# Kernel optimization log

Hardware: AMD Instinct MI355X
Metric: run time of the kernel (lower is better)

Reference implementation:

```python
import jax, jax.numpy as jnp
import numpy as np

N_INST = 1_000_000
N_BINS_X = 512
N_BINS_Y = 512
STDDEV_X = 0.6
STDDEV_Y = 0.6
STDDEV_TRUNC = 2.5
NUM_CKSR = 48
NUM_CE = 96
SLICE_CAP = 16
SQRT2 = float(np.sqrt(2.0))
# truncated window spans 2*trunc*stddev = 3.0 bin units -> at most 5 bins per axis
K = 5


def setup_inputs() -> dict:
    key = jax.random.key(0)
    k1, k2, k3, k4, k5 = jax.random.split(key, 5)
    scale = jnp.array([N_BINS_X, N_BINS_Y], dtype=jnp.float32)
    inst_pos = jax.random.uniform(k1, (N_INST, 2), dtype=jnp.float32) * scale
    luts = jax.random.randint(k2, (N_INST,), 0, 7, dtype=jnp.int32)
    luts = jnp.where(luts == 1, 0, luts)  # assert: no LUT has type 1
    ffs = jax.random.randint(k3, (N_INST,), 0, 2, dtype=jnp.int32)
    ffs = jnp.where(luts > 0, 0, ffs)  # an instance is either a LUT or a FF
    cksr = jax.random.randint(k4, (N_INST,), 0, NUM_CKSR, dtype=jnp.int32)
    ce = jax.random.randint(k5, (N_INST,), 0, NUM_CE, dtype=jnp.int32)
    ff_ctrlsets = jnp.stack([cksr, ce], axis=1)
    return {"inst_pos": inst_pos, "is_inst_luts": luts, "is_inst_ffs": ffs,
            "ff_ctrlsets": ff_ctrlsets}


def _axis_weights(pos, stddev, num_bins):
    """Truncated-Gaussian bin overlap weights along one axis.
    pos: (N,) centers in bin units. Returns bins (N,K) int32, weights (N,K)."""
    half = STDDEV_TRUNC * stddev
    lo_bin = jnp.floor(pos - half).astype(jnp.int32)            # (N,)
    bins = lo_bin[:, None] + jnp.arange(K, dtype=jnp.int32)     # (N,K)
    e_lo = bins.astype(pos.dtype)
    e_hi = e_lo + 1.0
    w_lo = (pos - half)[:, None]
    w_hi = (pos + half)[:, None]
    lo_c = jnp.clip(e_lo, w_lo, w_hi)
    hi_c = jnp.clip(e_hi, w_lo, w_hi)
    phi = lambda e: 0.5 * (1.0 + jax.lax.erf((e - pos[:, None]) / (stddev * SQRT2)))
    w = phi(hi_c) - phi(lo_c)
    valid = (bins >= 0) & (bins < num_bins)
    w = jnp.where(valid, w, 0.0)
    w = w / (jnp.sum(w, axis=1, keepdims=True) + 1e-12)  # each inst contributes unit demand
    return jnp.clip(bins, 0, num_bins - 1), w


def reference(inst_pos, is_inst_luts, is_inst_ffs, ff_ctrlsets):
    dt = inst_pos.dtype
    bx, wx = _axis_weights(inst_pos[:, 0], STDDEV_X, N_BINS_X)
    by, wy = _axis_weights(inst_pos[:, 1], STDDEV_Y, N_BINS_Y)
    w2 = wx[:, :, None] * wy[:, None, :]                        # (N,K,K)
    idx = bx[:, :, None] * N_BINS_Y + by[:, None, :]            # (N,K,K) flat bin id
    nb = N_BINS_X * N_BINS_Y

    lut_mask = is_inst_luts > 0
    ff_mask = (is_inst_ffs > 0) & (~lut_mask)

    # LUT demand map (Gaussian splat of LUT instances)
    lut_w = jnp.where(lut_mask[:, None, None], w2, 0.0)
    lut_dem = jnp.zeros(nb, dt).at[idx.reshape(-1)].add(lut_w.reshape(-1))

    # FF demand maps keyed by control sets (cksr shared per half-slice, ce per quarter)
    ff_w = jnp.where(ff_mask[:, None, None], w2, 0.0)
    cksr = ff_ctrlsets[:, 0]
    ce = ff_ctrlsets[:, 1]
    idx_ck = (idx * NUM_CKSR + cksr[:, None, None]).reshape(-1)
    idx_ce = (idx * NUM_CE + ce[:, None, None]).reshape(-1)
    ck_dem = jnp.zeros(nb * NUM_CKSR, dt).at[idx_ck].add(ff_w.reshape(-1))
    ck_dem = ck_dem.reshape(nb, NUM_CKSR)
    ce_dem = jnp.zeros(nb * NUM_CE, dt).at[idx_ce].add(ff_w.reshape(-1))
    ce_dem = ce_dem.reshape(nb, NUM_CE)

    # ultrascale packing rule: half-slice shares CK/SR, quarter-slice shares CE
    half_cap = SLICE_CAP / 2.0
    quarter_cap = SLICE_CAP / 4.0
    eff_ck = jnp.sum(jnp.ceil(ck_dem / half_cap), axis=1) * half_cap
    eff_ce = jnp.sum(jnp.ceil(ce_dem / quarter_cap), axis=1) * quarter_cap
    ff_eff = jnp.maximum(eff_ck, eff_ce)        # effective FF capacity consumed per bin
    ff_raw = jnp.sum(ck_dem, axis=1)            # raw FF demand per bin
    ff_scale = jnp.maximum(ff_eff / jnp.maximum(ff_raw, 1e-6), 1.0)
    lut_scale = jnp.maximum(lut_dem / SLICE_CAP, 1.0)

    # gather per-instance inflated resource area with the same Gaussian weights
    lut_area = jnp.sum(w2 * lut_scale[idx], axis=(1, 2))
    ff_area = jnp.sum(w2 * ff_scale[idx], axis=(1, 2))
    zero = jnp.zeros((), dt)
    return jnp.where(lut_mask, lut_area, zero) + jnp.where(ff_mask, ff_area, zero)
```

## Files before the change

kernel.cpp:

```cpp
#include <hip/hip_runtime.h>

#define N_INST   1000000
#define NBX      512
#define NBY      512
#define NB       (NBX * NBY)
#define NUM_CKSR 48
#define NUM_CE   96
#define K        4

#define FTX   16
#define FTY   8
#define TGX   (NBX / FTX)
#define TGY   (NBY / FTY)
#define NFT   (TGX * TGY)
#define CAPL  512
#define CAPF  256
#define RS    145
#define ACCW  (FTX * FTY * RS)
#define PXW   20
#define PYW   12

#define CSTRIDE 16

#define KHALF  ((float)(2.5 * 0.6))
#define KDENOM ((float)(0.6 * 1.4142135623730951))

__device__ __forceinline__ void axis_weights4(float pos, int nbins, int& lo_out, float w[K]) {
    float wlo = pos - KHALF;
    float whi = pos + KHALF;
    int lo_bin = (int)floorf(wlo);
    lo_out = lo_bin;
    float phi[K + 1];
#pragma unroll
    for (int k = 0; k <= K; ++k) {
        float e = (float)(lo_bin + k);
        float ec = fminf(fmaxf(e, wlo), whi);
        phi[k] = 0.5f * (1.f + erff((ec - pos) / KDENOM));
    }
    float wsum = 0.f;
#pragma unroll
    for (int k = 0; k < K; ++k) {
        int b = lo_bin + k;
        float ww = phi[k + 1] - phi[k];
        if (b < 0 || b >= nbins) ww = 0.f;
        w[k] = ww;
        wsum += ww;
    }
    float d = wsum + 1e-12f;
#pragma unroll
    for (int k = 0; k < K; ++k) w[k] = w[k] / d;
}

__global__ void __launch_bounds__(256) classify_kernel(
        const float* __restrict__ pos,
        const int* __restrict__ luts,
        const int* __restrict__ ffs,
        const int* __restrict__ ctrl,
        int* __restrict__ lut_cur,
        int* __restrict__ ff_cur,
        float2* __restrict__ lutb,
        uint4* __restrict__ ffb) {
    int i = blockIdx.x * blockDim.x + threadIdx.x;
    if (i >= N_INST) return;
    bool is_lut = luts[i] > 0;
    bool is_ff  = !is_lut && (ffs[i] > 0);
    if (!is_lut && !is_ff) return;

    float px = pos[2 * i], py = pos[2 * i + 1];

    if (is_lut) {
        int t = (((int)px) >> 4) * TGY + (((int)py) >> 3);
        int slot = atomicAdd(&lut_cur[t * CSTRIDE], 1);
        if (slot < CAPL) lutb[(size_t)t * CAPL + slot] = make_float2(px, py);
        return;
    }

    unsigned meta = (unsigned)ctrl[2 * i] | (((unsigned)ctrl[2 * i + 1] + 48u) << 8);
    uint4 entry = make_uint4(__float_as_uint(px), __float_as_uint(py), meta, 0u);
    int lox = (int)floorf(px - KHALF);
    int loy = (int)floorf(py - KHALF);
    int tx0 = max(lox, 0) >> 4, tx1 = min(lox + 3, NBX - 1) >> 4;
    int ty0 = max(loy, 0) >> 3, ty1 = min(loy + 3, NBY - 1) >> 3;
    for (int tx = tx0; tx <= tx1; ++tx) {
        for (int ty = ty0; ty <= ty1; ++ty) {
            int t = tx * TGY + ty;
            int slot = atomicAdd(&ff_cur[t * CSTRIDE], 1);
            if (slot < CAPF) ffb[(size_t)t * CAPF + slot] = entry;
        }
    }
}

__global__ void __launch_bounds__(1024) tile_kernel(
        const float2* __restrict__ lutb,
        const uint4* __restrict__ ffb,
        const int* __restrict__ lut_cur,
        const int* __restrict__ ff_cur,
        float* __restrict__ lut_dem,
        float* __restrict__ ff_scale) {
    __shared__ float acc[ACCW];
    __shared__ unsigned patch[PXW * PYW];
    int t = blockIdx.x;
    int X0 = (t / TGY) * FTX;
    int Y0 = (t % TGY) * FTY;
    int tid = threadIdx.x;

    for (int j = tid; j < ACCW; j += 1024) acc[j] = 0.f;
    if (tid < PXW * PYW) patch[tid] = 0u;
    __syncthreads();

    int nl = min(lut_cur[t * CSTRIDE], CAPL);
    for (int e = tid; e < nl; e += 1024) {
        float2 p = lutb[(size_t)t * CAPL + e];
        int lox, loy;
        float wx[K], wy[K];
        axis_weights4(p.x, NBX, lox, wx);
        axis_weights4(p.y, NBY, loy, wy);
        int base = (lox - (X0 - 2)) * PYW + (loy - (Y0 - 2));
#pragma unroll
        for (int kx = 0; kx < K; ++kx) {
            float wv = wx[kx] * 65536.f;
            int rb = base + kx * PYW;
#pragma unroll
            for (int ky = 0; ky < K; ++ky)
                atomicAdd(&patch[rb + ky], (unsigned)rintf(wv * wy[ky]));
        }
    }

    int nf = min(ff_cur[t * CSTRIDE], CAPF);
    for (int e = tid; e < nf; e += 1024) {
        uint4 a = ffb[(size_t)t * CAPF + e];
        float px = __uint_as_float(a.x);
        float py = __uint_as_float(a.y);
        int ck   = (int)(a.z & 255u);
        int ce48 = (int)((a.z >> 8) & 255u);
        int lox, loy;
        float wx[K], wy[K];
        axis_weights4(px, NBX, lox, wx);
        axis_weights4(py, NBY, loy, wy);
        int cx = lox - X0, cy = loy - Y0;
#pragma unroll
        for (int kx = 0; kx < K; ++kx) {
            int gx = cx + kx;
            if ((unsigned)gx >= FTX) continue;
            float wv = wx[kx];
#pragma unroll
            for (int ky = 0; ky < K; ++ky) {
                int gy = cy + ky;
                if ((unsigned)gy >= FTY) continue;
                float w2 = wv * wy[ky];
                if (w2 != 0.f) {
                    float* row = acc + (gx * FTY + gy) * RS;
                    unsafeAtomicAdd(row + ck, w2);
                    unsafeAtomicAdd(row + ce48, w2);
                }
            }
        }
    }
    __syncthreads();

    if (tid < 512) {
        int lb = tid >> 2, q = tid & 3;
        const float* row = acc + lb * RS;
        float raw = 0.f, effck = 0.f, effce = 0.f;
#pragma unroll
        for (int c = 0; c < 12; ++c) {
            float v = row[12 * q + c];
            raw += v;
            effck += ceilf(v * 0.125f);
        }
#pragma unroll
        for (int c = 0; c < 24; ++c) {
            effce += ceilf(row[48 + 24 * q + c] * 0.25f);
        }
        raw   += __shfl_xor(raw, 1);   raw   += __shfl_xor(raw, 2);
        effck += __shfl_xor(effck, 1); effck += __shfl_xor(effck, 2);
        effce += __shfl_xor(effce, 1); effce += __shfl_xor(effce, 2);
        if (q == 0) {
            float eff = fmaxf(effck * 8.f, effce * 4.f);
            int gx = X0 + (lb >> 3);
            int gy = Y0 + (lb & 7);
            ff_scale[gx * NBY + gy] = fmaxf(eff / fmaxf(raw, 1e-6f), 1.f);
        }
    } else if (tid < 512 + PXW * PYW) {
        int j = tid - 512;
        unsigned v = patch[j];
        if (v != 0u) {
            int gx = X0 - 2 + j / PYW;
            int gy = Y0 - 2 + j % PYW;
            if (gx >= 0 && gx < NBX && gy >= 0 && gy < NBY)
                unsafeAtomicAdd(&lut_dem[gx * NBY + gy], (float)v * (1.f / 65536.f));
        }
    }
}

__global__ void __launch_bounds__(256) area_kernel(
        const float* __restrict__ pos,
        const int* __restrict__ luts,
        const int* __restrict__ ffs,
        const float* __restrict__ lut_dem,
        const float* __restrict__ ff_scale,
        float* __restrict__ out) {
    int i = blockIdx.x * blockDim.x + threadIdx.x;
    if (i >= N_INST) return;
    bool is_lut = luts[i] > 0;
    bool is_ff  = (ffs[i] > 0) && !is_lut;
    if (!is_lut && !is_ff) { out[i] = 0.f; return; }

    float px = pos[2 * i], py = pos[2 * i + 1];
    int lox, loy;
    float wx[K], wy[K];
    axis_weights4(px, NBX, lox, wx);
    axis_weights4(py, NBY, loy, wy);

    const float* tbl = is_lut ? lut_dem : ff_scale;
    float acc = 0.f;
#pragma unroll
    for (int kx = 0; kx < K; ++kx) {
        int gx = min(max(lox + kx, 0), NBX - 1);
#pragma unroll
        for (int ky = 0; ky < K; ++ky) {
            int gy = min(max(loy + ky, 0), NBY - 1);
            float w2 = wx[kx] * wy[ky];
            float v = tbl[gx * NBY + gy];
            float sc = is_lut ? fmaxf(v * 0.0625f, 1.f) : v;
            acc += w2 * sc;
        }
    }
    out[i] = acc;
}

extern "C" void kernel_launch(void* const* d_in, const int* in_sizes, int n_in,
                              void* d_out, int out_size, void* d_ws, size_t ws_size,
                              hipStream_t stream) {
    const float* pos  = (const float*)d_in[0];
    const int*   luts = (const int*)d_in[1];
    const int*   ffs  = (const int*)d_in[2];
    const int*   ctrl = (const int*)d_in[3];
    float* out = (float*)d_out;

    int*    lut_cur  = (int*)d_ws;
    int*    ff_cur   = lut_cur + NFT * CSTRIDE;
    float*  lut_dem  = (float*)(ff_cur + NFT * CSTRIDE);
    float*  ff_scale = lut_dem + NB;
    float2* lutb     = (float2*)(ff_scale + NB);
    uint4*  ffb      = (uint4*)(lutb + (size_t)NFT * CAPL);

    hipMemsetAsync(d_ws, 0, (size_t)(2 * NFT * CSTRIDE + NB) * sizeof(int), stream);

    dim3 blk(256);
    dim3 grdI((N_INST + 255) / 256);

    classify_kernel<<<grdI, blk, 0, stream>>>(pos, luts, ffs, ctrl,
                                              lut_cur, ff_cur, lutb, ffb);
    tile_kernel<<<NFT, dim3(1024), 0, stream>>>(lutb, ffb, lut_cur, ff_cur,
                                                lut_dem, ff_scale);
    area_kernel<<<grdI, blk, 0, stream>>>(pos, luts, ffs, lut_dem, ff_scale, out);
}
```

Before: 135.4 us.

## Split per-tile bucket counters into sub-buckets to reduce atomic contention

Each tile's LUT and FF bucket is split into 8 sub-buckets selected by block index, so the classify atomics spread across more counters. The tile kernel builds a prefix over sub-bucket counts and maps each flat index back to its sub-bucket. This adds a larger memset, a serial prefix computation and per-element lookup overhead, and risks overflow with the smaller per-sub-bucket capacities.

```diff
diff --git a/kernel.cpp b/kernel.cpp
--- a/kernel.cpp
+++ b/kernel.cpp
@@ -13,8 +13,9 @@
 #define TGX   (NBX / FTX)
 #define TGY   (NBY / FTY)
 #define NFT   (TGX * TGY)
-#define CAPL  512
-#define CAPF  256
+#define SUB   8
+#define CAPL  96
+#define CAPF  48
 #define RS    145
 #define ACCW  (FTX * FTY * RS)
 #define PXW   20
@@ -62,6 +63,7 @@
         uint4* __restrict__ ffb) {
     int i = blockIdx.x * blockDim.x + threadIdx.x;
     if (i >= N_INST) return;
+    int sb = blockIdx.x & (SUB - 1);
     bool is_lut = luts[i] > 0;
     bool is_ff  = !is_lut && (ffs[i] > 0);
     if (!is_lut && !is_ff) return;
@@ -70,8 +72,9 @@
 
     if (is_lut) {
         int t = (((int)px) >> 4) * TGY + (((int)py) >> 3);
-        int slot = atomicAdd(&lut_cur[t * CSTRIDE], 1);
-        if (slot < CAPL) lutb[(size_t)t * CAPL + slot] = make_float2(px, py);
+        int sbk = t * SUB + sb;
+        int slot = atomicAdd(&lut_cur[sbk * CSTRIDE], 1);
+        if (slot < CAPL) lutb[(size_t)sbk * CAPL + slot] = make_float2(px, py);
         return;
     }
 
@@ -83,9 +86,9 @@
     int ty0 = max(loy, 0) >> 3, ty1 = min(loy + 3, NBY - 1) >> 3;
     for (int tx = tx0; tx <= tx1; ++tx) {
         for (int ty = ty0; ty <= ty1; ++ty) {
-            int t = tx * TGY + ty;
-            int slot = atomicAdd(&ff_cur[t * CSTRIDE], 1);
-            if (slot < CAPF) ffb[(size_t)t * CAPF + slot] = entry;
+            int sbk = (tx * TGY + ty) * SUB + sb;
+            int slot = atomicAdd(&ff_cur[sbk * CSTRIDE], 1);
+            if (slot < CAPF) ffb[(size_t)sbk * CAPF + slot] = entry;
         }
     }
 }
@@ -99,6 +102,7 @@
         float* __restrict__ ff_scale) {
     __shared__ float acc[ACCW];
     __shared__ unsigned patch[PXW * PYW];
+    __shared__ int lpre[SUB + 1], fpre[SUB + 1];
     int t = blockIdx.x;
     int X0 = (t / TGY) * FTX;
     int Y0 = (t % TGY) * FTY;
@@ -106,11 +110,21 @@
 
     for (int j = tid; j < ACCW; j += 1024) acc[j] = 0.f;
     if (tid < PXW * PYW) patch[tid] = 0u;
+    if (tid == 0) {
+        int s = 0; lpre[0] = 0;
+        for (int c = 0; c < SUB; ++c) { s += min(lut_cur[(t * SUB + c) * CSTRIDE], CAPL); lpre[c + 1] = s; }
+    } else if (tid == 1) {
+        int s = 0; fpre[0] = 0;
+        for (int c = 0; c < SUB; ++c) { s += min(ff_cur[(t * SUB + c) * CSTRIDE], CAPF); fpre[c + 1] = s; }
+    }
     __syncthreads();
 
-    int nl = min(lut_cur[t * CSTRIDE], CAPL);
-    for (int e = tid; e < nl; e += 1024) {
-        float2 p = lutb[(size_t)t * CAPL + e];
+    int ltot = lpre[SUB];
+    for (int e = tid; e < ltot; e += 1024) {
+        int c = 0;
+#pragma unroll
+        for (int k = 1; k < SUB; ++k) c += (e >= lpre[k]);
+        float2 p = lutb[((size_t)t * SUB + c) * CAPL + (e - lpre[c])];
         int lox, loy;
         float wx[K], wy[K];
         axis_weights4(p.x, NBX, lox, wx);
@@ -126,9 +140,12 @@
         }
     }
 
-    int nf = min(ff_cur[t * CSTRIDE], CAPF);
-    for (int e = tid; e < nf; e += 1024) {
-        uint4 a = ffb[(size_t)t * CAPF + e];
+    int ftot = fpre[SUB];
+    for (int e = tid; e < ftot; e += 1024) {
+        int c = 0;
+#pragma unroll
+        for (int k = 1; k < SUB; ++k) c += (e >= fpre[k]);
+        uint4 a = ffb[((size_t)t * SUB + c) * CAPF + (e - fpre[c])];
         float px = __uint_as_float(a.x);
         float py = __uint_as_float(a.y);
         int ck   = (int)(a.z & 255u);
@@ -239,13 +256,13 @@
     float* out = (float*)d_out;
 
     int*    lut_cur  = (int*)d_ws;
-    int*    ff_cur   = lut_cur + NFT * CSTRIDE;
-    float*  lut_dem  = (float*)(ff_cur + NFT * CSTRIDE);
+    int*    ff_cur   = lut_cur + NFT * SUB * CSTRIDE;
+    float*  lut_dem  = (float*)(ff_cur + NFT * SUB * CSTRIDE);
     float*  ff_scale = lut_dem + NB;
     float2* lutb     = (float2*)(ff_scale + NB);
-    uint4*  ffb      = (uint4*)(lutb + (size_t)NFT * CAPL);
-
-    hipMemsetAsync(d_ws, 0, (size_t)(2 * NFT * CSTRIDE + NB) * sizeof(int), stream);
+    uint4*  ffb      = (uint4*)(lutb + (size_t)NFT * SUB * CAPL);
+
+    hipMemsetAsync(d_ws, 0, (size_t)(2 * NFT * SUB * CSTRIDE + NB) * sizeof(int), stream);
 
     dim3 blk(256);
     dim3 grdI((N_INST + 255) / 256);
```

New measurement: 133.7 us. Within noise of the previous version (-1.3%).
